# Kernel optimization log

Measured on AMD Instinct MI355X. Metric: run time of the kernel, lower is better.

Reference implementation:

```python
import jax, jax.numpy as jnp
import numpy as np

B, T, E, H, A = 64, 1024, 512, 512, 512  # batch, src_len, enc_dim, hidden, attention_dim
D_IN = 512                                # decoder input embedding dim; cell input = D_IN + E


def setup_inputs() -> dict:
    key = jax.random.key(0)
    ks = jax.random.split(key, 10)
    s = 0.05  # small init to keep tanh/sigmoid unsaturated
    return {
        "inputs":  jax.random.normal(ks[0], (B, D_IN), jnp.float32),
        "states":  jax.random.normal(ks[1], (B, H), jnp.float32),
        "encoded": jax.random.normal(ks[2], (B, T, E), jnp.float32),
        "W_enc":   jax.random.normal(ks[3], (E, A), jnp.float32) * s,
        "W_state": jax.random.normal(ks[4], (H, A), jnp.float32) * s,
        "v":       jax.random.normal(ks[5], (A,), jnp.float32) * s,
        "W_ih":    jax.random.normal(ks[6], (3 * H, D_IN + E), jnp.float32) * s,
        "W_hh":    jax.random.normal(ks[7], (3 * H, H), jnp.float32) * s,
        "b_ih":    jnp.zeros((3 * H,), jnp.float32),
        "b_hh":    jnp.zeros((3 * H,), jnp.float32),
    }


def reference(inputs, states, encoded, W_enc, W_state, v, W_ih, W_hh, b_ih, b_hh):
    # --- Bahdanau additive attention (one decoder step) ---
    enc_proj = jnp.einsum("bte,ea->bta", encoded, W_enc)      # setup_memory projection
    st_proj = states @ W_state                                  # [B,A]
    scores = jnp.tanh(enc_proj + st_proj[:, None, :]) @ v       # [B,T]
    weights = jax.nn.softmax(scores, axis=-1)                   # [B,T]
    context = jnp.einsum("bt,bte->be", weights, encoded)       # [B,E]

    # --- GRU cell step on concat(inputs, context) (torch.nn.GRUCell math) ---
    x = jnp.concatenate([inputs, context], axis=-1)             # [B, D_IN+E]
    gi = x @ W_ih.T + b_ih                                      # [B, 3H]
    gh = states @ W_hh.T + b_hh                                 # [B, 3H]
    i_r, i_z, i_n = jnp.split(gi, 3, axis=-1)
    h_r, h_z, h_n = jnp.split(gh, 3, axis=-1)
    r = jax.nn.sigmoid(i_r + h_r)
    z = jax.nn.sigmoid(i_z + h_z)
    n = jnp.tanh(i_n + r * h_n)
    return (1.0 - z) * n + z * states                           # [B,H]
```

## Files before the change

kernel.cpp:

```cpp
#include <hip/hip_runtime.h>
#include <hip/hip_bf16.h>

#define BN   64
#define TN   1024
#define EN   512
#define AN   512
#define HN   512
#define G3H  1536

typedef __bf16 bf16x8 __attribute__((ext_vector_type(8)));
typedef __bf16 bf16x4 __attribute__((ext_vector_type(4)));
typedef float  f32x8  __attribute__((ext_vector_type(8)));
typedef float  f32x4  __attribute__((ext_vector_type(4)));
typedef unsigned int uint4v __attribute__((ext_vector_type(4)));

__device__ __forceinline__ float fast_tanh(float x) {
    float e = __expf(2.0f * x);
    return 1.0f - 2.0f / (e + 1.0f);
}
__device__ __forceinline__ float fast_sigmoid(float x) {
    return 1.0f / (1.0f + __expf(-x));
}

#define GL2LDS16(gsrc, ldst)                                                  \
    __builtin_amdgcn_global_load_lds(                                         \
        (const __attribute__((address_space(1))) unsigned int*)(gsrc),        \
        (__attribute__((address_space(3))) unsigned int*)(ldst), 16, 0, 0)

__global__ __launch_bounds__(256) void prep_kernel(
    const float* __restrict__ states, const float* __restrict__ W_enc,
    const float* __restrict__ W_state, const float* __restrict__ inputs,
    const float* __restrict__ W_ih, const float* __restrict__ W_hh,
    float* __restrict__ stp, __bf16* __restrict__ wencT,
    __bf16* __restrict__ xbf, __bf16* __restrict__ stbf,
    __bf16* __restrict__ wihbf, __bf16* __restrict__ whhbf,
    float* __restrict__ scores)
{
    __shared__ float srow[512];
    int blk = blockIdx.x, tid = threadIdx.x;

    if (blk < 64) {
        int b = blk;
        srow[tid] = states[b * 512 + tid];
        srow[tid + 256] = states[b * 512 + tid + 256];
        __syncthreads();
        int n0 = tid, n1 = tid + 256;
        float a0 = 0.f, a1 = 0.f;
        for (int k = 0; k < 512; ++k) {
            float s = srow[k];
            a0 += s * W_state[k * 512 + n0];
            a1 += s * W_state[k * 512 + n1];
        }
        stp[b * 512 + n0] = a0;
        stp[b * 512 + n1] = a1;
    } else if (blk < 72) {
        int n = (blk - 64) * 64 + (tid & 63);
        int cseg = tid >> 6;
        for (int c = cseg * 16; c < cseg * 16 + 16; ++c) {
            f32x8 f;
            #pragma unroll
            for (int j = 0; j < 8; ++j) f[j] = W_enc[(c * 8 + j) * 512 + n];
            int cs = (c & ~7) | ((c & 7) ^ (n & 7));
            *(bf16x8*)(wencT + n * 512 + cs * 8) = __builtin_convertvector(f, bf16x8);
        }
    } else if (blk < 840) {
        int base4 = (blk - 72) * 512 + tid * 2;
        #pragma unroll
        for (int j = 0; j < 2; ++j) {
            int i4 = base4 + j;
            f32x4 f = *(const f32x4*)(W_ih + i4 * 4);
            *(bf16x4*)(wihbf + i4 * 4) = __builtin_convertvector(f, bf16x4);
        }
    } else if (blk < 1224) {
        int base4 = (blk - 840) * 512 + tid * 2;
        #pragma unroll
        for (int j = 0; j < 2; ++j) {
            int i4 = base4 + j;
            f32x4 f = *(const f32x4*)(W_hh + i4 * 4);
            *(bf16x4*)(whhbf + i4 * 4) = __builtin_convertvector(f, bf16x4);
        }
    } else if (blk < 1240) {
        int base4 = (blk - 1224) * 512 + tid * 2;
        #pragma unroll
        for (int j = 0; j < 2; ++j) {
            int i4 = base4 + j;
            int e = i4 * 4;
            int b = e >> 9, c = e & 511;
            f32x4 f = *(const f32x4*)(inputs + e);
            *(bf16x4*)(xbf + b * 1024 + c) = __builtin_convertvector(f, bf16x4);
        }
    } else if (blk < 1256) {
        int base4 = (blk - 1240) * 512 + tid * 2;
        #pragma unroll
        for (int j = 0; j < 2; ++j) {
            int i4 = base4 + j;
            int e = i4 * 4;
            f32x4 f = *(const f32x4*)(states + e);
            *(bf16x4*)(stbf + e) = __builtin_convertvector(f, bf16x4);
        }
    } else {
        int e = (blk - 1256) * 1024 + tid * 4;
        *(f32x4*)(scores + e) = (f32x4){0.f, 0.f, 0.f, 0.f};
    }
}

__global__ __launch_bounds__(256, 4) void score_kernel(
    const float* __restrict__ enc, const __bf16* __restrict__ wencT,
    const float* __restrict__ stp, const float* __restrict__ v,
    float* __restrict__ scores)
{
    __shared__ __align__(16) __bf16 As[128 * 64];
    __shared__ __align__(16) __bf16 Bs[128 * 64];
    __shared__ float sacc[256];

    int tid = threadIdx.x;
    int bid = blockIdx.x;
    int orig = (bid & 7) * 256 + (bid >> 3);
    int rt = orig >> 2, ct = orig & 3;
    int grow0 = rt * 128;
    int c0 = ct * 128;
    int b = grow0 >> 10;

    int lane = tid & 63, wid = tid >> 6;
    int wrow = wid >> 1, wcol = wid & 1;
    int l15 = lane & 15, g = lane >> 4;

    f32x4 acc[4][4];
    #pragma unroll
    for (int m = 0; m < 4; ++m)
        #pragma unroll
        for (int n = 0; n < 4; ++n) acc[m][n] = (f32x4){0.f, 0.f, 0.f, 0.f};

    for (int ks = 0; ks < 8; ++ks) {
        f32x8 aR[4];
        #pragma unroll
        for (int i = 0; i < 4; ++i) {
            int p = i * 256 + tid;
            int row = p >> 3, c = p & 7;
            aR[i] = *(const f32x8*)(enc + (size_t)(grow0 + row) * 512 + ks * 64 + c * 8);
        }
        #pragma unroll
        for (int i = 0; i < 4; ++i) {
            int p = i * 256 + tid;
            int row = p >> 3, c = p & 7;
            const __bf16* src = wencT + (size_t)(c0 + row) * 512 + ks * 64 + c * 8;
            char* dst = (char*)Bs + (i * 256 + wid * 64) * 16;
            GL2LDS16(src, dst);
        }
        #pragma unroll
        for (int i = 0; i < 4; ++i) {
            int p = i * 256 + tid;
            int row = p >> 3, c = p & 7;
            int cs = c ^ (row & 7);
            *(bf16x8*)((char*)As + row * 128 + cs * 16) =
                __builtin_convertvector(aR[i], bf16x8);
        }
        __syncthreads();
        #pragma unroll
        for (int kk = 0; kk < 2; ++kk) {
            bf16x8 af[4], bfr[4];
            #pragma unroll
            for (int m = 0; m < 4; ++m) {
                int row = wrow * 64 + m * 16 + l15;
                int cch = (kk * 4 + g) ^ (row & 7);
                af[m] = *(const bf16x8*)((char*)As + row * 128 + cch * 16);
            }
            #pragma unroll
            for (int n = 0; n < 4; ++n) {
                int row = wcol * 64 + n * 16 + l15;
                int cch = (kk * 4 + g) ^ (row & 7);
                bfr[n] = *(const bf16x8*)((char*)Bs + row * 128 + cch * 16);
            }
            #pragma unroll
            for (int m = 0; m < 4; ++m)
                #pragma unroll
                for (int n = 0; n < 4; ++n)
                    acc[m][n] = __builtin_amdgcn_mfma_f32_16x16x32_bf16(
                        af[m], bfr[n], acc[m][n], 0, 0, 0);
        }
        if (ks < 7) __syncthreads();
    }

    float sv[4], vw[4];
    #pragma unroll
    for (int n = 0; n < 4; ++n) {
        int col = c0 + wcol * 64 + n * 16 + l15;
        sv[n] = stp[b * 512 + col];
        vw[n] = v[col];
    }
    float rp[16];
    #pragma unroll
    for (int i = 0; i < 16; ++i) rp[i] = 0.f;
    #pragma unroll
    for (int m = 0; m < 4; ++m)
        #pragma unroll
        for (int n = 0; n < 4; ++n) {
            #pragma unroll
            for (int r = 0; r < 4; ++r)
                rp[m * 4 + r] += vw[n] * fast_tanh(acc[m][n][r] + sv[n]);
        }
    #pragma unroll
    for (int i = 0; i < 16; ++i) {
        rp[i] += __shfl_xor(rp[i], 1);
        rp[i] += __shfl_xor(rp[i], 2);
        rp[i] += __shfl_xor(rp[i], 4);
        rp[i] += __shfl_xor(rp[i], 8);
    }
    if (l15 == 0) {
        #pragma unroll
        for (int m = 0; m < 4; ++m)
            #pragma unroll
            for (int r = 0; r < 4; ++r)
                sacc[wcol * 128 + wrow * 64 + m * 16 + g * 4 + r] = rp[m * 4 + r];
    }
    __syncthreads();
    if (tid < 128)
        atomicAdd(scores + grow0 + tid, sacc[tid] + sacc[128 + tid]);
}

__global__ __launch_bounds__(256) void ctx_kernel(
    const float* __restrict__ scores, const float* __restrict__ enc,
    __bf16* __restrict__ xbf)
{
    __shared__ float wsm[1024];
    __shared__ float red[512];
    __shared__ float tmp[8];
    int tid = threadIdx.x, lane = tid & 63, w = tid >> 6;
    int b = blockIdx.x >> 2, c0 = (blockIdx.x & 3) * 128;

    f32x4 s = *(const f32x4*)(scores + b * 1024 + tid * 4);
    float m = fmaxf(fmaxf(s[0], s[1]), fmaxf(s[2], s[3]));
    #pragma unroll
    for (int off = 32; off >= 1; off >>= 1) m = fmaxf(m, __shfl_xor(m, off));
    if (lane == 0) tmp[w] = m;
    __syncthreads();
    float M = fmaxf(fmaxf(tmp[0], tmp[1]), fmaxf(tmp[2], tmp[3]));
    float e0 = __expf(s[0] - M), e1 = __expf(s[1] - M);
    float e2 = __expf(s[2] - M), e3 = __expf(s[3] - M);
    wsm[tid * 4 + 0] = e0; wsm[tid * 4 + 1] = e1;
    wsm[tid * 4 + 2] = e2; wsm[tid * 4 + 3] = e3;
    float sum = e0 + e1 + e2 + e3;
    #pragma unroll
    for (int off = 32; off >= 1; off >>= 1) sum += __shfl_xor(sum, off);
    if (lane == 0) tmp[4 + w] = sum;
    __syncthreads();
    float S = tmp[4] + tmp[5] + tmp[6] + tmp[7];

    const float* ep = enc + ((b * 1024 + w * 256) * 512 + c0 + lane * 2);
    float ax = 0.f, ay = 0.f;
    #pragma unroll 4
    for (int t = 0; t < 256; ++t) {
        float wt = wsm[w * 256 + t];
        float2 ev = *(const float2*)(ep + t * 512);
        ax += wt * ev.x;
        ay += wt * ev.y;
    }
    red[w * 128 + lane * 2] = ax;
    red[w * 128 + lane * 2 + 1] = ay;
    __syncthreads();
    if (tid < 128) {
        float c = (red[tid] + red[128 + tid] + red[256 + tid] + red[384 + tid]) / S;
        xbf[b * 1024 + 512 + c0 + tid] = (__bf16)c;
    }
}

__global__ __launch_bounds__(256) void gru_gemm(
    const __bf16* __restrict__ xbf, const __bf16* __restrict__ stbf,
    const __bf16* __restrict__ wihbf, const __bf16* __restrict__ whhbf,
    const float* __restrict__ b_ih, const float* __restrict__ b_hh,
    float* __restrict__ gi, float* __restrict__ gh)
{
    __shared__ __align__(16) __bf16 As[64 * 72];
    __shared__ __align__(16) __bf16 Bs[128 * 72];
    int blk = blockIdx.x, tid = threadIdx.x;
    bool is_gh = blk >= 12;
    int n0 = (is_gh ? blk - 12 : blk) * 128;
    int K = is_gh ? 512 : 1024;
    const __bf16* Aptr = is_gh ? stbf : xbf;
    const __bf16* Bptr = is_gh ? whhbf : wihbf;
    const float* bias = is_gh ? b_hh : b_ih;
    float* outp = is_gh ? gh : gi;

    int lane = tid & 63, wid = tid >> 6, l15 = lane & 15, g = lane >> 4;
    f32x4 acc[4][2];
    #pragma unroll
    for (int i = 0; i < 4; ++i)
        #pragma unroll
        for (int j = 0; j < 2; ++j) acc[i][j] = (f32x4){0.f, 0.f, 0.f, 0.f};

    int nkc = K >> 6;
    for (int kc = 0; kc < nkc; ++kc) {
        int k0 = kc * 64;
        #pragma unroll
        for (int q = 0; q < 2; ++q) {
            int ch = tid * 2 + q, row = ch >> 3, seg = ch & 7;
            uint4v u = *(const uint4v*)(Aptr + row * K + k0 + seg * 8);
            *(uint4v*)(As + row * 72 + seg * 8) = u;
        }
        #pragma unroll
        for (int q = 0; q < 4; ++q) {
            int ch = tid * 4 + q, row = ch >> 3, seg = ch & 7;
            uint4v u = *(const uint4v*)(Bptr + (n0 + row) * K + k0 + seg * 8);
            *(uint4v*)(Bs + row * 72 + seg * 8) = u;
        }
        __syncthreads();
        #pragma unroll
        for (int kk = 0; kk < 2; ++kk) {
            bf16x8 af[4], bfr[2];
            #pragma unroll
            for (int m = 0; m < 4; ++m)
                af[m] = *(const bf16x8*)(As + (m * 16 + l15) * 72 + kk * 32 + g * 8);
            #pragma unroll
            for (int n = 0; n < 2; ++n)
                bfr[n] = *(const bf16x8*)(Bs + (wid * 32 + n * 16 + l15) * 72 + kk * 32 + g * 8);
            #pragma unroll
            for (int m = 0; m < 4; ++m)
                #pragma unroll
                for (int n = 0; n < 2; ++n)
                    acc[m][n] = __builtin_amdgcn_mfma_f32_16x16x32_bf16(
                        af[m], bfr[n], acc[m][n], 0, 0, 0);
        }
        __syncthreads();
    }
    #pragma unroll
    for (int m = 0; m < 4; ++m)
        #pragma unroll
        for (int n = 0; n < 2; ++n) {
            int col = n0 + wid * 32 + n * 16 + l15;
            float bb = bias[col];
            #pragma unroll
            for (int r = 0; r < 4; ++r) {
                int brow = m * 16 + g * 4 + r;
                outp[brow * 1536 + col] = acc[m][n][r] + bb;
            }
        }
}

__global__ __launch_bounds__(256) void gru_gates(
    const float* __restrict__ gi, const float* __restrict__ gh,
    const float* __restrict__ states, float* __restrict__ out)
{
    int i = blockIdx.x * 256 + threadIdx.x;
    int b = i >> 9, j = i & 511;
    const float* gib = gi + b * 1536;
    const float* ghb = gh + b * 1536;
    float r = fast_sigmoid(gib[j] + ghb[j]);
    float z = fast_sigmoid(gib[512 + j] + ghb[512 + j]);
    float n = fast_tanh(gib[1024 + j] + r * ghb[1024 + j]);
    out[i] = (1.f - z) * n + z * states[i];
}

extern "C" void kernel_launch(void* const* d_in, const int* in_sizes, int n_in,
                              void* d_out, int out_size, void* d_ws, size_t ws_size,
                              hipStream_t stream)
{
    const float* inputs  = (const float*)d_in[0];
    const float* states  = (const float*)d_in[1];
    const float* encoded = (const float*)d_in[2];
    const float* W_enc   = (const float*)d_in[3];
    const float* W_state = (const float*)d_in[4];
    const float* v       = (const float*)d_in[5];
    const float* W_ih    = (const float*)d_in[6];
    const float* W_hh    = (const float*)d_in[7];
    const float* b_ih    = (const float*)d_in[8];
    const float* b_hh    = (const float*)d_in[9];
    float* out = (float*)d_out;
    char* ws = (char*)d_ws;

    float*  stp    = (float*)(ws + 0);
    __bf16* wencT  = (__bf16*)(ws + 131072);
    float*  scores = (float*)(ws + 655360);
    __bf16* xbf    = (__bf16*)(ws + 917504);
    __bf16* stbf   = (__bf16*)(ws + 1048576);
    __bf16* wihbf  = (__bf16*)(ws + 1114112);
    __bf16* whhbf  = (__bf16*)(ws + 4259840);
    float*  gi     = (float*)(ws + 5832704);
    float*  gh     = (float*)(ws + 6225920);

    prep_kernel<<<1320, 256, 0, stream>>>(states, W_enc, W_state, inputs, W_ih, W_hh,
                                          stp, wencT, xbf, stbf, wihbf, whhbf, scores);
    score_kernel<<<2048, 256, 0, stream>>>(encoded, wencT, stp, v, scores);
    ctx_kernel<<<256, 256, 0, stream>>>(scores, encoded, xbf);
    gru_gemm<<<24, 256, 0, stream>>>(xbf, stbf, wihbf, whhbf, b_ih, b_hh, gi, gh);
    gru_gates<<<128, 256, 0, stream>>>(gi, gh, states, out);
}
```

Measured before the change: 126.3 us.

## Fuse softmax-weighted context into score kernel via last-block counters

Removes the separate ctx_kernel. The last of the four column-tile blocks for each row tile now finishes that tile. It exponentiates its 128 scores and adds them to a per-batch sum. It then accumulates the weighted encoder rows into a float context buffer with atomics while that tile is likely still cached. The GRU GEMM normalises the context by the per-batch sum while loading it and converts it to bf16. This avoids a second full read of the encoder tensor from memory and one kernel launch. The cost is more atomics, a softmax with no max subtraction that could overflow for larger scores, and extra zero-initialisation in prep.

```diff
diff --git a/kernel.cpp b/kernel.cpp
--- a/kernel.cpp
+++ b/kernel.cpp
@@ -34,7 +34,8 @@
     float* __restrict__ stp, __bf16* __restrict__ wencT,
     __bf16* __restrict__ xbf, __bf16* __restrict__ stbf,
     __bf16* __restrict__ wihbf, __bf16* __restrict__ whhbf,
-    float* __restrict__ scores)
+    float* __restrict__ scores, float* __restrict__ ctxacc,
+    float* __restrict__ wsum, int* __restrict__ cnt)
 {
     __shared__ float srow[512];
     int blk = blockIdx.x, tid = threadIdx.x;
@@ -98,20 +99,29 @@
             f32x4 f = *(const f32x4*)(states + e);
             *(bf16x4*)(stbf + e) = __builtin_convertvector(f, bf16x4);
         }
-    } else {
+    } else if (blk < 1320) {
         int e = (blk - 1256) * 1024 + tid * 4;
         *(f32x4*)(scores + e) = (f32x4){0.f, 0.f, 0.f, 0.f};
+    } else if (blk < 1352) {
+        int e = (blk - 1320) * 1024 + tid * 4;
+        *(f32x4*)(ctxacc + e) = (f32x4){0.f, 0.f, 0.f, 0.f};
+    } else {
+        if (tid < 64) wsum[tid] = 0.f;
+        if (tid < 128) *(f32x4*)((float*)cnt + tid * 4) = (f32x4){0.f, 0.f, 0.f, 0.f};
     }
 }
 
 __global__ __launch_bounds__(256, 4) void score_kernel(
     const float* __restrict__ enc, const __bf16* __restrict__ wencT,
     const float* __restrict__ stp, const float* __restrict__ v,
-    float* __restrict__ scores)
+    float* __restrict__ scores, float* __restrict__ ctxacc,
+    float* __restrict__ wsum, int* __restrict__ cnt)
 {
     __shared__ __align__(16) __bf16 As[128 * 64];
     __shared__ __align__(16) __bf16 Bs[128 * 64];
     __shared__ float sacc[256];
+    __shared__ float wls[128];
+    __shared__ int amLast;
 
     int tid = threadIdx.x;
     int bid = blockIdx.x;
@@ -216,51 +226,39 @@
     __syncthreads();
     if (tid < 128)
         atomicAdd(scores + grow0 + tid, sacc[tid] + sacc[128 + tid]);
-}
-
-__global__ __launch_bounds__(256) void ctx_kernel(
-    const float* __restrict__ scores, const float* __restrict__ enc,
-    __bf16* __restrict__ xbf)
-{
-    __shared__ float wsm[1024];
-    __shared__ float red[512];
-    __shared__ float tmp[8];
-    int tid = threadIdx.x, lane = tid & 63, w = tid >> 6;
-    int b = blockIdx.x >> 2, c0 = (blockIdx.x & 3) * 128;
-
-    f32x4 s = *(const f32x4*)(scores + b * 1024 + tid * 4);
-    float m = fmaxf(fmaxf(s[0], s[1]), fmaxf(s[2], s[3]));
-    #pragma unroll
-    for (int off = 32; off >= 1; off >>= 1) m = fmaxf(m, __shfl_xor(m, off));
-    if (lane == 0) tmp[w] = m;
+
+    __threadfence();
     __syncthreads();
-    float M = fmaxf(fmaxf(tmp[0], tmp[1]), fmaxf(tmp[2], tmp[3]));
-    float e0 = __expf(s[0] - M), e1 = __expf(s[1] - M);
-    float e2 = __expf(s[2] - M), e3 = __expf(s[3] - M);
-    wsm[tid * 4 + 0] = e0; wsm[tid * 4 + 1] = e1;
-    wsm[tid * 4 + 2] = e2; wsm[tid * 4 + 3] = e3;
-    float sum = e0 + e1 + e2 + e3;
-    #pragma unroll
-    for (int off = 32; off >= 1; off >>= 1) sum += __shfl_xor(sum, off);
-    if (lane == 0) tmp[4 + w] = sum;
+    if (tid == 0) {
+        int old = atomicAdd(cnt + rt, 1);
+        amLast = (old == 3);
+    }
     __syncthreads();
-    float S = tmp[4] + tmp[5] + tmp[6] + tmp[7];
-
-    const float* ep = enc + ((b * 1024 + w * 256) * 512 + c0 + lane * 2);
-    float ax = 0.f, ay = 0.f;
-    #pragma unroll 4
-    for (int t = 0; t < 256; ++t) {
-        float wt = wsm[w * 256 + t];
-        float2 ev = *(const float2*)(ep + t * 512);
-        ax += wt * ev.x;
-        ay += wt * ev.y;
-    }
-    red[w * 128 + lane * 2] = ax;
-    red[w * 128 + lane * 2 + 1] = ay;
-    __syncthreads();
-    if (tid < 128) {
-        float c = (red[tid] + red[128 + tid] + red[256 + tid] + red[384 + tid]) / S;
-        xbf[b * 1024 + 512 + c0 + tid] = (__bf16)c;
+    if (amLast) {
+        float w = 0.f;
+        if (tid < 128) {
+            float s = __hip_atomic_load(scores + grow0 + tid,
+                                        __ATOMIC_ACQUIRE, __HIP_MEMORY_SCOPE_AGENT);
+            w = __expf(s);
+            wls[tid] = w;
+        }
+        if (wid < 2) {
+            #pragma unroll
+            for (int off = 32; off >= 1; off >>= 1) w += __shfl_xor(w, off);
+            if (lane == 0) atomicAdd(wsum + b, w);
+        }
+        __syncthreads();
+        const float* ep = enc + (size_t)grow0 * 512 + tid * 2;
+        float ax = 0.f, ay = 0.f;
+        #pragma unroll 4
+        for (int t = 0; t < 128; ++t) {
+            float wt = wls[t];
+            float2 ev = *(const float2*)(ep + (size_t)t * 512);
+            ax += wt * ev.x;
+            ay += wt * ev.y;
+        }
+        atomicAdd(ctxacc + b * 512 + tid * 2, ax);
+        atomicAdd(ctxacc + b * 512 + tid * 2 + 1, ay);
     }
 }
 
@@ -268,6 +266,7 @@
     const __bf16* __restrict__ xbf, const __bf16* __restrict__ stbf,
     const __bf16* __restrict__ wihbf, const __bf16* __restrict__ whhbf,
     const float* __restrict__ b_ih, const float* __restrict__ b_hh,
+    const float* __restrict__ ctxacc, const float* __restrict__ wsum,
     float* __restrict__ gi, float* __restrict__ gh)
 {
     __shared__ __align__(16) __bf16 As[64 * 72];
@@ -276,12 +275,21 @@
     bool is_gh = blk >= 12;
     int n0 = (is_gh ? blk - 12 : blk) * 128;
     int K = is_gh ? 512 : 1024;
-    const __bf16* Aptr = is_gh ? stbf : xbf;
     const __bf16* Bptr = is_gh ? whhbf : wihbf;
     const float* bias = is_gh ? b_hh : b_ih;
     float* outp = is_gh ? gh : gi;
 
     int lane = tid & 63, wid = tid >> 6, l15 = lane & 15, g = lane >> 4;
+
+    float rinvq[2];
+    if (!is_gh) {
+        #pragma unroll
+        for (int q = 0; q < 2; ++q) {
+            int row = (tid * 2 + q) >> 3;
+            rinvq[q] = 1.0f / wsum[row];
+        }
+    }
+
     f32x4 acc[4][2];
     #pragma unroll
     for (int i = 0; i < 4; ++i)
@@ -291,11 +299,30 @@
     int nkc = K >> 6;
     for (int kc = 0; kc < nkc; ++kc) {
         int k0 = kc * 64;
-        #pragma unroll
-        for (int q = 0; q < 2; ++q) {
-            int ch = tid * 2 + q, row = ch >> 3, seg = ch & 7;
-            uint4v u = *(const uint4v*)(Aptr + row * K + k0 + seg * 8);
-            *(uint4v*)(As + row * 72 + seg * 8) = u;
+        if (is_gh) {
+            #pragma unroll
+            for (int q = 0; q < 2; ++q) {
+                int ch = tid * 2 + q, row = ch >> 3, seg = ch & 7;
+                uint4v u = *(const uint4v*)(stbf + row * 512 + k0 + seg * 8);
+                *(uint4v*)(As + row * 72 + seg * 8) = u;
+            }
+        } else if (k0 < 512) {
+            #pragma unroll
+            for (int q = 0; q < 2; ++q) {
+                int ch = tid * 2 + q, row = ch >> 3, seg = ch & 7;
+                uint4v u = *(const uint4v*)(xbf + row * 1024 + k0 + seg * 8);
+                *(uint4v*)(As + row * 72 + seg * 8) = u;
+            }
+        } else {
+            #pragma unroll
+            for (int q = 0; q < 2; ++q) {
+                int ch = tid * 2 + q, row = ch >> 3, seg = ch & 7;
+                f32x8 f = *(const f32x8*)(ctxacc + row * 512 + (k0 - 512) + seg * 8);
+                f32x8 fs;
+                #pragma unroll
+                for (int j = 0; j < 8; ++j) fs[j] = f[j] * rinvq[q];
+                *(bf16x8*)(As + row * 72 + seg * 8) = __builtin_convertvector(fs, bf16x8);
+            }
         }
         #pragma unroll
         for (int q = 0; q < 4; ++q) {
@@ -376,11 +403,16 @@
     __bf16* whhbf  = (__bf16*)(ws + 4259840);
     float*  gi     = (float*)(ws + 5832704);
     float*  gh     = (float*)(ws + 6225920);
-
-    prep_kernel<<<1320, 256, 0, stream>>>(states, W_enc, W_state, inputs, W_ih, W_hh,
-                                          stp, wencT, xbf, stbf, wihbf, whhbf, scores);
-    score_kernel<<<2048, 256, 0, stream>>>(encoded, wencT, stp, v, scores);
-    ctx_kernel<<<256, 256, 0, stream>>>(scores, encoded, xbf);
-    gru_gemm<<<24, 256, 0, stream>>>(xbf, stbf, wihbf, whhbf, b_ih, b_hh, gi, gh);
+    float*  ctxacc = (float*)(ws + 6619136);
+    float*  wsum   = (float*)(ws + 6750208);
+    int*    cnt    = (int*)  (ws + 6750464);
+
+    prep_kernel<<<1353, 256, 0, stream>>>(states, W_enc, W_state, inputs, W_ih, W_hh,
+                                          stp, wencT, xbf, stbf, wihbf, whhbf,
+                                          scores, ctxacc, wsum, cnt);
+    score_kernel<<<2048, 256, 0, stream>>>(encoded, wencT, stp, v,
+                                           scores, ctxacc, wsum, cnt);
+    gru_gemm<<<24, 256, 0, stream>>>(xbf, stbf, wihbf, whhbf, b_ih, b_hh,
+                                     ctxacc, wsum, gi, gh);
     gru_gates<<<128, 256, 0, stream>>>(gi, gh, states, out);
 }
```

Measured after the change: 335.8 us. +165.8%, slower.

## Pre-convert encoder to swizzled bf16 buffer shared by score and context kernels

Applied to the files above, without the earlier changes.

Adds a conversion kernel that writes the fp32 encoder tensor once as bf16 with the LDS swizzle already applied. The score kernel can then load its A tiles straight from global into LDS, like its B tiles, with no register staging or in-kernel conversion. The context kernel reads the bf16 copy with 16-byte vector loads and reduces across lane groups with shuffles. This halves the encoder bytes each consumer reads, but adds a full fp32 read plus a bf16 write (about 128MB fp32 in, 64MB out), an extra launch, and bf16 rounding in the context sum.

```diff
diff --git a/kernel.cpp b/kernel.cpp
--- a/kernel.cpp
+++ b/kernel.cpp
@@ -104,8 +104,24 @@
     }
 }
 
+__global__ __launch_bounds__(256) void cvt_kernel(
+    const float* __restrict__ enc, __bf16* __restrict__ encbf)
+{
+    size_t row0 = (size_t)blockIdx.x * 8;
+    int tid = threadIdx.x;
+    #pragma unroll
+    for (int i = 0; i < 2; ++i) {
+        int p = i * 256 + tid;
+        int r = p >> 6, c = p & 63;
+        size_t row = row0 + r;
+        f32x8 f = *(const f32x8*)(enc + row * 512 + c * 8);
+        int cs = (c & ~7) | ((c & 7) ^ (int)(row & 7));
+        *(bf16x8*)(encbf + row * 512 + cs * 8) = __builtin_convertvector(f, bf16x8);
+    }
+}
+
 __global__ __launch_bounds__(256, 4) void score_kernel(
-    const float* __restrict__ enc, const __bf16* __restrict__ wencT,
+    const __bf16* __restrict__ encbf, const __bf16* __restrict__ wencT,
     const float* __restrict__ stp, const float* __restrict__ v,
     float* __restrict__ scores)
 {
@@ -132,12 +148,13 @@
         for (int n = 0; n < 4; ++n) acc[m][n] = (f32x4){0.f, 0.f, 0.f, 0.f};
 
     for (int ks = 0; ks < 8; ++ks) {
-        f32x8 aR[4];
         #pragma unroll
         for (int i = 0; i < 4; ++i) {
             int p = i * 256 + tid;
             int row = p >> 3, c = p & 7;
-            aR[i] = *(const f32x8*)(enc + (size_t)(grow0 + row) * 512 + ks * 64 + c * 8);
+            const __bf16* src = encbf + (size_t)(grow0 + row) * 512 + ks * 64 + c * 8;
+            char* dst = (char*)As + (i * 256 + wid * 64) * 16;
+            GL2LDS16(src, dst);
         }
         #pragma unroll
         for (int i = 0; i < 4; ++i) {
@@ -147,14 +164,6 @@
             char* dst = (char*)Bs + (i * 256 + wid * 64) * 16;
             GL2LDS16(src, dst);
         }
-        #pragma unroll
-        for (int i = 0; i < 4; ++i) {
-            int p = i * 256 + tid;
-            int row = p >> 3, c = p & 7;
-            int cs = c ^ (row & 7);
-            *(bf16x8*)((char*)As + row * 128 + cs * 16) =
-                __builtin_convertvector(aR[i], bf16x8);
-        }
         __syncthreads();
         #pragma unroll
         for (int kk = 0; kk < 2; ++kk) {
@@ -219,11 +228,11 @@
 }
 
 __global__ __launch_bounds__(256) void ctx_kernel(
-    const float* __restrict__ scores, const float* __restrict__ enc,
+    const float* __restrict__ scores, const __bf16* __restrict__ encbf,
     __bf16* __restrict__ xbf)
 {
     __shared__ float wsm[1024];
-    __shared__ float red[512];
+    __shared__ float red[4][128];
     __shared__ float tmp[8];
     int tid = threadIdx.x, lane = tid & 63, w = tid >> 6;
     int b = blockIdx.x >> 2, c0 = (blockIdx.x & 3) * 128;
@@ -246,20 +255,32 @@
     __syncthreads();
     float S = tmp[4] + tmp[5] + tmp[6] + tmp[7];
 
-    const float* ep = enc + ((b * 1024 + w * 256) * 512 + c0 + lane * 2);
-    float ax = 0.f, ay = 0.f;
-    #pragma unroll 4
-    for (int t = 0; t < 256; ++t) {
-        float wt = wsm[w * 256 + t];
-        float2 ev = *(const float2*)(ep + t * 512);
-        ax += wt * ev.x;
-        ay += wt * ev.y;
-    }
-    red[w * 128 + lane * 2] = ax;
-    red[w * 128 + lane * 2 + 1] = ay;
+    int q = lane >> 4, li = lane & 15;
+    int ch0 = (c0 >> 3) + li;
+    float a[8];
+    #pragma unroll
+    for (int k = 0; k < 8; ++k) a[k] = 0.f;
+    const __bf16* ebase = encbf + (size_t)(b * 1024) * 512;
+    for (int j = 0; j < 64; ++j) {
+        int t = w * 256 + q + 4 * j;
+        float wt = wsm[t];
+        int chw = (ch0 & ~7) | ((ch0 & 7) ^ (t & 7));
+        bf16x8 ev = *(const bf16x8*)(ebase + (size_t)t * 512 + chw * 8);
+        #pragma unroll
+        for (int k = 0; k < 8; ++k) a[k] += wt * (float)ev[k];
+    }
+    #pragma unroll
+    for (int k = 0; k < 8; ++k) {
+        a[k] += __shfl_xor(a[k], 16);
+        a[k] += __shfl_xor(a[k], 32);
+    }
+    if (lane < 16) {
+        #pragma unroll
+        for (int k = 0; k < 8; ++k) red[w][li * 8 + k] = a[k];
+    }
     __syncthreads();
     if (tid < 128) {
-        float c = (red[tid] + red[128 + tid] + red[256 + tid] + red[384 + tid]) / S;
+        float c = (red[0][tid] + red[1][tid] + red[2][tid] + red[3][tid]) / S;
         xbf[b * 1024 + 512 + c0 + tid] = (__bf16)c;
     }
 }
@@ -376,11 +397,13 @@
     __bf16* whhbf  = (__bf16*)(ws + 4259840);
     float*  gi     = (float*)(ws + 5832704);
     float*  gh     = (float*)(ws + 6225920);
+    __bf16* encbf  = (__bf16*)(ws + 6619136);
 
     prep_kernel<<<1320, 256, 0, stream>>>(states, W_enc, W_state, inputs, W_ih, W_hh,
                                           stp, wencT, xbf, stbf, wihbf, whhbf, scores);
-    score_kernel<<<2048, 256, 0, stream>>>(encoded, wencT, stp, v, scores);
-    ctx_kernel<<<256, 256, 0, stream>>>(scores, encoded, xbf);
+    cvt_kernel<<<8192, 256, 0, stream>>>(encoded, encbf);
+    score_kernel<<<2048, 256, 0, stream>>>(encbf, wencT, stp, v, scores);
+    ctx_kernel<<<256, 256, 0, stream>>>(scores, encbf, xbf);
     gru_gemm<<<24, 256, 0, stream>>>(xbf, stbf, wihbf, whhbf, b_ih, b_hh, gi, gh);
     gru_gates<<<128, 256, 0, stream>>>(gi, gh, states, out);
 }
```

After: 140.5 us. 1.11x slower.
